# Performance work log

Measured on AMD Instinct MI355X. Metric: run time of the kernel, lower is better.

Reference implementation:

```python
import jax, jax.numpy as jnp
import numpy as np

B, N, D = 2, 2048, 1024
H = 16
HD = D // H
SCALE = HD ** -0.5


def setup_inputs() -> dict:
    key = jax.random.key(0)
    k1, k2, kw, kb = jax.random.split(key, 4)
    x1 = jax.random.normal(k1, (B, N, D), dtype=jnp.float32)
    x2 = jax.random.normal(k2, (B, N, D), dtype=jnp.float32)
    # fused qkv linear: torch nn.Linear(dim, 3*dim): W [3D, D], b [3D]
    bound = 1.0 / np.sqrt(D)
    qkv_w = jax.random.uniform(kw, (3 * D, D), minval=-bound, maxval=bound, dtype=jnp.float32)
    qkv_b = jax.random.uniform(kb, (3 * D,), minval=-bound, maxval=bound, dtype=jnp.float32)
    return {"x1": x1, "x2": x2, "qkv_w": qkv_w, "qkv_b": qkv_b}


def reference(x1, x2, qkv_w, qkv_b):
    # qkv projections (only q from x1 and k,v from x2 are used by the module)
    q1 = (jnp.einsum('bnd,ed->bne', x1, qkv_w[:D]) + qkv_b[:D])
    k2 = (jnp.einsum('bnd,ed->bne', x2, qkv_w[D:2 * D]) + qkv_b[D:2 * D])
    v2 = (jnp.einsum('bnd,ed->bne', x2, qkv_w[2 * D:]) + qkv_b[2 * D:])
    # [B, H, N, HD]
    q1 = q1.reshape(B, N, H, HD).transpose(0, 2, 1, 3)
    k2 = k2.reshape(B, N, H, HD).transpose(0, 2, 1, 3)
    v2 = v2.reshape(B, N, H, HD).transpose(0, 2, 1, 3)
    # explicit QK^T -> softmax -> AV (materializes [B,H,N,N] like the original)
    scores = jnp.einsum('bhqd,bhkd->bhqk', q1, k2) * SCALE
    attn = jax.nn.softmax(scores, axis=-1)
    out = jnp.einsum('bhqk,bhkd->bhqd', attn, v2)
    # [B, N, D]; note original module skips out_proj (never applied in forward)
    return out.transpose(0, 2, 1, 3).reshape(B, N, D)
```

## Files before the change

kernel.cpp:

```cpp
#include <hip/hip_runtime.h>
#include <cstdint>
#include <cstddef>

#define B_   2
#define N_   2048
#define D_   1024
#define H_   16
#define HD_  64
#define QSCALE_ 0.18033688011112042f

typedef unsigned short u16;
typedef unsigned int   u32;
typedef __attribute__((ext_vector_type(8))) short short8;
typedef __attribute__((ext_vector_type(4))) float f32x4;
typedef __attribute__((ext_vector_type(16))) float f32x16;
typedef __attribute__((ext_vector_type(4))) float fl4;
typedef __attribute__((ext_vector_type(4))) unsigned short us4;
typedef __attribute__((ext_vector_type(4))) unsigned int u32x4;

#if __has_builtin(__builtin_amdgcn_exp2f)
#define EXP2F(x) __builtin_amdgcn_exp2f(x)
#else
#define EXP2F(x) exp2f(x)
#endif

__device__ __forceinline__ u16 f2bf(float f) {
  u32 u = __builtin_bit_cast(u32, f);
  u += 0x7fffu + ((u >> 16) & 1u);
  return (u16)(u >> 16);
}

__device__ __forceinline__ u32 cvtpk(float lo, float hi) {
  u32 r;
  asm("v_cvt_pk_bf16_f32 %0, %1, %2" : "=v"(r) : "v"(lo), "v"(hi));
  return r;
}

__device__ __forceinline__ void plswap(u32& a, u32& b) {
  asm volatile("v_permlane32_swap_b32 %0, %1" : "+v"(a), "+v"(b));
}

__device__ __forceinline__ void gload16(const void* g, void* l) {
  typedef __attribute__((address_space(1))) unsigned int gu32;
  typedef __attribute__((address_space(3))) unsigned int lu32;
  __builtin_amdgcn_global_load_lds((gu32*)g, (lu32*)l, 16, 0, 0);
}

__global__ void convert_kernel(const fl4* __restrict__ x1, const fl4* __restrict__ x2,
                               const fl4* __restrict__ w,
                               us4* __restrict__ o1, us4* __restrict__ o2,
                               us4* __restrict__ ow) {
  const int NX = (B_ * N_ * D_) / 4;
  const int NW = (3 * D_ * D_) / 4;
  int stride = gridDim.x * blockDim.x;
  for (int i = blockIdx.x * blockDim.x + threadIdx.x; i < NX; i += stride) {
    fl4 a = x1[i];
    us4 r; r.x = f2bf(a.x); r.y = f2bf(a.y); r.z = f2bf(a.z); r.w = f2bf(a.w);
    o1[i] = r;
    fl4 b = x2[i];
    us4 s; s.x = f2bf(b.x); s.y = f2bf(b.y); s.z = f2bf(b.z); s.w = f2bf(b.w);
    o2[i] = s;
    if (i < NW) {
      fl4 c = w[i];
      us4 t; t.x = f2bf(c.x); t.y = f2bf(c.y); t.z = f2bf(c.z); t.w = f2bf(c.w);
      ow[i] = t;
    }
  }
}

__global__ __launch_bounds__(256) void qkv_gemm(
    const u16* __restrict__ x1b, const u16* __restrict__ x2b,
    const u16* __restrict__ wb, const float* __restrict__ bias,
    u16* __restrict__ Qb, u16* __restrict__ Kb, u16* __restrict__ Vtb) {
  const int z = blockIdx.z;
  const u16* X = (z == 0) ? x1b : x2b;
  const u16* W = wb + (size_t)z * D_ * D_;
  const float* bz = bias + z * D_;
  const int m0 = blockIdx.y * 128;
  const int e0 = blockIdx.x * 128;
  const int tid = threadIdx.x;
  const int lane = tid & 63;
  const int w = tid >> 6;
  const int wr = w >> 1, wc = w & 1;
  const int col = lane & 15, quad = lane >> 4;

  __shared__ __align__(16) u16 As[128 * 32];
  __shared__ __align__(16) u16 Bs[128 * 32];

  f32x4 acc[4][4] = {};

  int off0 = w * 2048 + lane * 16;
  int row0 = off0 >> 6;
  int ke0  = (off0 & 63) >> 1;
  int off1 = off0 + 1024;
  int row1 = off1 >> 6;
  int ke1  = (off1 & 63) >> 1;

  const u16* gA0 = X + (size_t)(m0 + row0) * D_ + ke0;
  const u16* gA1 = X + (size_t)(m0 + row1) * D_ + ke1;
  const u16* gB0 = W + (size_t)(e0 + row0) * D_ + ke0;
  const u16* gB1 = W + (size_t)(e0 + row1) * D_ + ke1;
  u16* lA0 = &As[w * 1024];
  u16* lA1 = &As[w * 1024 + 512];
  u16* lB0 = &Bs[w * 1024];
  u16* lB1 = &Bs[w * 1024 + 512];

  for (int k0 = 0; k0 < D_; k0 += 32) {
    __syncthreads();
    gload16(gA0 + k0, lA0);
    gload16(gA1 + k0, lA1);
    gload16(gB0 + k0, lB0);
    gload16(gB1 + k0, lB1);
    __syncthreads();

    short8 a[4], b[4];
#pragma unroll
    for (int i = 0; i < 4; ++i)
      a[i] = *(const short8*)&As[(wr * 64 + i * 16 + col) * 32 + quad * 8];
#pragma unroll
    for (int j = 0; j < 4; ++j)
      b[j] = *(const short8*)&Bs[(wc * 64 + j * 16 + col) * 32 + quad * 8];
#pragma unroll
    for (int i = 0; i < 4; ++i)
#pragma unroll
      for (int j = 0; j < 4; ++j)
        acc[i][j] = __builtin_amdgcn_mfma_f32_16x16x32_bf16(a[i], b[j], acc[i][j], 0, 0, 0);
  }

#pragma unroll
  for (int j = 0; j < 4; ++j) {
    int eg = e0 + wc * 64 + j * 16 + col;
    float bj = bz[eg];
    int h = eg >> 6, d = eg & 63;
#pragma unroll
    for (int i = 0; i < 4; ++i) {
#pragma unroll
      for (int r = 0; r < 4; ++r) {
        int m = m0 + wr * 64 + i * 16 + quad * 4 + r;
        int bb = m >> 11, n = m & (N_ - 1);
        float v = acc[i][j][r] + bj;
        if (z == 0) v *= QSCALE_;
        u16 o = f2bf(v);
        if (z == 0)      Qb [(((size_t)bb * H_ + h) * N_ + n) * HD_ + d] = o;
        else if (z == 1) Kb [(((size_t)bb * H_ + h) * N_ + n) * HD_ + d] = o;
        else             Vtb[(((size_t)bb * H_ + h) * HD_ + d) * N_ + n] = o;
      }
    }
  }
}

__global__ __launch_bounds__(256, 2) void attn_kernel(
    const u16* __restrict__ Qb, const u16* __restrict__ Kb,
    const u16* __restrict__ Vtb, float* __restrict__ out) {
  const int bh = blockIdx.y;
  const int bb = bh >> 4, h = bh & 15;
  const int q0 = blockIdx.x * 128;
  const int tid = threadIdx.x;
  const int lane = tid & 63;
  const int w = tid >> 6;
  const int l31 = lane & 31, hf = lane >> 5, r7 = lane & 7;

  const u16* __restrict__ Q  = Qb  + ((size_t)bh << 17);
  const u16* __restrict__ K  = Kb  + ((size_t)bh << 17);
  const u16* __restrict__ Vt = Vtb + ((size_t)bh << 17);

  __shared__ __align__(16) u16 Ks[2][64 * 64];
  __shared__ __align__(16) u16 Vs[2][64 * 64];
  __shared__ float Ls[4][32];

  const u16* Qr = Q + (size_t)(q0 + w * 32 + l31) * HD_;
  short8 qf[4];
#pragma unroll
  for (int c = 0; c < 4; ++c)
    qf[c] = *(const short8*)&Qr[c * 16 + hf * 8];

  const int srow = tid >> 3;
  const int sg   = tid & 7;
  const int lw0 = srow * 64 + ((sg ^ (srow & 7)) * 8);
  const int lw1 = lw0 + 2048;
  const u16* gK = K + tid * 8;
  const u16* gV = Vt + srow * N_ + sg * 8;

  f32x16 accO[2] = {};
  float lsum = 0.f;

  short8 kA = *(const short8*)(gK);
  short8 kB = *(const short8*)(gK + 2048);
  short8 vA = *(const short8*)(gV);
  short8 vB = *(const short8*)(gV + 32 * N_);
  *(short8*)&Ks[0][lw0] = kA;
  *(short8*)&Ks[0][lw1] = kB;
  *(short8*)&Vs[0][lw0] = vA;
  *(short8*)&Vs[0][lw1] = vB;

  for (int t = 0; t < N_ / 64; ++t) {
    __syncthreads();
    const int cur = t & 1;
    if (t < N_ / 64 - 1) {
      const int k0n = (t + 1) * 64;
      kA = *(const short8*)(gK + k0n * 64);
      kB = *(const short8*)(gK + k0n * 64 + 2048);
      vA = *(const short8*)(gV + k0n);
      vB = *(const short8*)(gV + k0n + 32 * N_);
    }
    const u16* Kc = Ks[cur];
    const u16* Vc = Vs[cur];

    f32x16 sT[2] = {};
    __builtin_amdgcn_s_setprio(1);
#pragma unroll
    for (int kb = 0; kb < 2; ++kb) {
      const int rb = (kb * 32 + l31) * 64;
#pragma unroll
      for (int c = 0; c < 4; ++c) {
        short8 kf = *(const short8*)&Kc[rb + (((c * 2 + hf) ^ r7) * 8)];
        sT[kb] = __builtin_amdgcn_mfma_f32_32x32x16_bf16(kf, qf[c], sT[kb], 0, 0, 0);
      }
    }
    __builtin_amdgcn_s_setprio(0);

#pragma unroll
    for (int kb = 0; kb < 2; ++kb)
#pragma unroll
      for (int i = 0; i < 16; ++i) {
        float e = EXP2F(sT[kb][i]);
        lsum += e;
        sT[kb][i] = e;
      }

    short8 pf[4];
#pragma unroll
    for (int kc = 0; kc < 4; ++kc) {
      const int kb = kc >> 1, o = (kc & 1) * 8;
      u32 X = cvtpk(sT[kb][o + 0], sT[kb][o + 1]);
      u32 Y = cvtpk(sT[kb][o + 4], sT[kb][o + 5]);
      plswap(X, Y);
      u32 Z = cvtpk(sT[kb][o + 2], sT[kb][o + 3]);
      u32 W = cvtpk(sT[kb][o + 6], sT[kb][o + 7]);
      plswap(Z, W);
      u32x4 pw = {X, Z, Y, W};
      pf[kc] = __builtin_bit_cast(short8, pw);
    }

    __builtin_amdgcn_s_setprio(1);
#pragma unroll
    for (int db = 0; db < 2; ++db) {
      const int rb = (db * 32 + l31) * 64;
#pragma unroll
      for (int kc = 0; kc < 4; ++kc) {
        short8 vf = *(const short8*)&Vc[rb + (((kc * 2 + hf) ^ r7) * 8)];
        accO[db] = __builtin_amdgcn_mfma_f32_32x32x16_bf16(pf[kc], vf, accO[db], 0, 0, 0);
      }
    }
    __builtin_amdgcn_s_setprio(0);

    if (t < N_ / 64 - 1) {
      u16* Kn = (u16*)Ks[cur ^ 1];
      u16* Vn = (u16*)Vs[cur ^ 1];
      *(short8*)&Kn[lw0] = kA;
      *(short8*)&Kn[lw1] = kB;
      *(short8*)&Vn[lw0] = vA;
      *(short8*)&Vn[lw1] = vB;
    }
  }

  lsum += __shfl_xor(lsum, 32);
  if (hf == 0) Ls[w][l31] = 1.0f / lsum;
  __syncthreads();

  float rinv[16];
#pragma unroll
  for (int r = 0; r < 16; ++r)
    rinv[r] = Ls[w][(r & 3) + 8 * (r >> 2) + 4 * hf];

#pragma unroll
  for (int db = 0; db < 2; ++db)
#pragma unroll
    for (int r = 0; r < 16; ++r) {
      int n = q0 + w * 32 + (r & 3) + 8 * (r >> 2) + 4 * hf;
      int e = h * HD_ + db * 32 + l31;
      out[((size_t)bb * N_ + n) * D_ + e] = accO[db][r] * rinv[r];
    }
}

extern "C" void kernel_launch(void* const* d_in, const int* in_sizes, int n_in,
                              void* d_out, int out_size, void* d_ws, size_t ws_size,
                              hipStream_t stream) {
  const float* x1 = (const float*)d_in[0];
  const float* x2 = (const float*)d_in[1];
  const float* qw = (const float*)d_in[2];
  const float* qb = (const float*)d_in[3];
  float* out = (float*)d_out;

  u16* ws   = (u16*)d_ws;
  u16* x1b  = ws;
  u16* x2b  = ws + 4194304;
  u16* wb   = ws + 8388608;
  u16* Qbf  = ws + 11534336;
  u16* Kbf  = ws + 15728640;
  u16* Vtb  = ws + 19922944;
  if (ws_size < (size_t)24117248 * 2) return;

  convert_kernel<<<dim3(1024), dim3(256), 0, stream>>>(
      (const fl4*)x1, (const fl4*)x2, (const fl4*)qw,
      (us4*)x1b, (us4*)x2b, (us4*)wb);

  qkv_gemm<<<dim3(8, 32, 3), dim3(256), 0, stream>>>(
      x1b, x2b, wb, qb, Qbf, Kbf, Vtb);

  attn_kernel<<<dim3(16, 32), dim3(256), 0, stream>>>(Qbf, Kbf, Vtb, out);
}
```

Measured before the change: 172.1 us.

## Fuse fp32-to-bf16 conversion into QKV GEMM with register-staged double buffering

Removes the separate convert kernel and has the QKV GEMM read fp32 inputs and weights directly. Each tile is converted to bf16 in registers and written into a double-buffered LDS tile, with the next tile's global loads issued before the current MFMAs, and MFMA priority is raised via s_setprio. This drops a kernel launch and the write and re-read of the bf16 copies, and shrinks the workspace. In exchange each GEMM block now reads twice the bytes (fp32) and repeats the conversion for every tile reuse across blocks, and it replaces the async global_load_lds path with register staging.

```diff
diff --git a/kernel.cpp b/kernel.cpp
--- a/kernel.cpp
+++ b/kernel.cpp
@@ -36,45 +36,23 @@
   return r;
 }
 
+__device__ __forceinline__ short8 pack8(fl4 lo, fl4 hi) {
+  u32x4 r = { cvtpk(lo.x, lo.y), cvtpk(lo.z, lo.w),
+              cvtpk(hi.x, hi.y), cvtpk(hi.z, hi.w) };
+  return __builtin_bit_cast(short8, r);
+}
+
 __device__ __forceinline__ void plswap(u32& a, u32& b) {
   asm volatile("v_permlane32_swap_b32 %0, %1" : "+v"(a), "+v"(b));
 }
 
-__device__ __forceinline__ void gload16(const void* g, void* l) {
-  typedef __attribute__((address_space(1))) unsigned int gu32;
-  typedef __attribute__((address_space(3))) unsigned int lu32;
-  __builtin_amdgcn_global_load_lds((gu32*)g, (lu32*)l, 16, 0, 0);
-}
-
-__global__ void convert_kernel(const fl4* __restrict__ x1, const fl4* __restrict__ x2,
-                               const fl4* __restrict__ w,
-                               us4* __restrict__ o1, us4* __restrict__ o2,
-                               us4* __restrict__ ow) {
-  const int NX = (B_ * N_ * D_) / 4;
-  const int NW = (3 * D_ * D_) / 4;
-  int stride = gridDim.x * blockDim.x;
-  for (int i = blockIdx.x * blockDim.x + threadIdx.x; i < NX; i += stride) {
-    fl4 a = x1[i];
-    us4 r; r.x = f2bf(a.x); r.y = f2bf(a.y); r.z = f2bf(a.z); r.w = f2bf(a.w);
-    o1[i] = r;
-    fl4 b = x2[i];
-    us4 s; s.x = f2bf(b.x); s.y = f2bf(b.y); s.z = f2bf(b.z); s.w = f2bf(b.w);
-    o2[i] = s;
-    if (i < NW) {
-      fl4 c = w[i];
-      us4 t; t.x = f2bf(c.x); t.y = f2bf(c.y); t.z = f2bf(c.z); t.w = f2bf(c.w);
-      ow[i] = t;
-    }
-  }
-}
-
 __global__ __launch_bounds__(256) void qkv_gemm(
-    const u16* __restrict__ x1b, const u16* __restrict__ x2b,
-    const u16* __restrict__ wb, const float* __restrict__ bias,
+    const float* __restrict__ x1, const float* __restrict__ x2,
+    const float* __restrict__ qw, const float* __restrict__ bias,
     u16* __restrict__ Qb, u16* __restrict__ Kb, u16* __restrict__ Vtb) {
   const int z = blockIdx.z;
-  const u16* X = (z == 0) ? x1b : x2b;
-  const u16* W = wb + (size_t)z * D_ * D_;
+  const float* X = (z == 0) ? x1 : x2;
+  const float* W = qw + (size_t)z * D_ * D_;
   const float* bz = bias + z * D_;
   const int m0 = blockIdx.y * 128;
   const int e0 = blockIdx.x * 128;
@@ -84,48 +62,64 @@
   const int wr = w >> 1, wc = w & 1;
   const int col = lane & 15, quad = lane >> 4;
 
-  __shared__ __align__(16) u16 As[128 * 32];
-  __shared__ __align__(16) u16 Bs[128 * 32];
+  __shared__ __align__(16) u16 As[2][128 * 32];
+  __shared__ __align__(16) u16 Bs[2][128 * 32];
 
   f32x4 acc[4][4] = {};
 
-  int off0 = w * 2048 + lane * 16;
-  int row0 = off0 >> 6;
-  int ke0  = (off0 & 63) >> 1;
-  int off1 = off0 + 1024;
-  int row1 = off1 >> 6;
-  int ke1  = (off1 & 63) >> 1;
-
-  const u16* gA0 = X + (size_t)(m0 + row0) * D_ + ke0;
-  const u16* gA1 = X + (size_t)(m0 + row1) * D_ + ke1;
-  const u16* gB0 = W + (size_t)(e0 + row0) * D_ + ke0;
-  const u16* gB1 = W + (size_t)(e0 + row1) * D_ + ke1;
-  u16* lA0 = &As[w * 1024];
-  u16* lA1 = &As[w * 1024 + 512];
-  u16* lB0 = &Bs[w * 1024];
-  u16* lB1 = &Bs[w * 1024 + 512];
-
-  for (int k0 = 0; k0 < D_; k0 += 32) {
+  const int srow = tid >> 2;
+  const int seg  = tid & 3;
+  const float* gA0 = X + (size_t)(m0 + srow) * D_ + seg * 8;
+  const float* gA1 = X + (size_t)(m0 + 64 + srow) * D_ + seg * 8;
+  const float* gB0 = W + (size_t)(e0 + srow) * D_ + seg * 8;
+  const float* gB1 = W + (size_t)(e0 + 64 + srow) * D_ + seg * 8;
+  const int ls0 = srow * 32 + seg * 8;
+  const int ls1 = (srow + 64) * 32 + seg * 8;
+
+  fl4 aal, aah, abl, abh, bal, bah, bbl, bbh;
+
+#define LOADT(k0)                                                     \
+  do {                                                                \
+    aal = *(const fl4*)(gA0 + (k0)); aah = *(const fl4*)(gA0 + (k0) + 4); \
+    abl = *(const fl4*)(gA1 + (k0)); abh = *(const fl4*)(gA1 + (k0) + 4); \
+    bal = *(const fl4*)(gB0 + (k0)); bah = *(const fl4*)(gB0 + (k0) + 4); \
+    bbl = *(const fl4*)(gB1 + (k0)); bbh = *(const fl4*)(gB1 + (k0) + 4); \
+  } while (0)
+#define STORET(buf)                                                   \
+  do {                                                                \
+    *(short8*)&As[buf][ls0] = pack8(aal, aah);                        \
+    *(short8*)&As[buf][ls1] = pack8(abl, abh);                        \
+    *(short8*)&Bs[buf][ls0] = pack8(bal, bah);                        \
+    *(short8*)&Bs[buf][ls1] = pack8(bbl, bbh);                        \
+  } while (0)
+
+  LOADT(0);
+  STORET(0);
+
+  for (int t = 0; t < D_ / 32; ++t) {
     __syncthreads();
-    gload16(gA0 + k0, lA0);
-    gload16(gA1 + k0, lA1);
-    gload16(gB0 + k0, lB0);
-    gload16(gB1 + k0, lB1);
-    __syncthreads();
+    const int cur = t & 1;
+    if (t < D_ / 32 - 1) LOADT((t + 1) * 32);
 
     short8 a[4], b[4];
 #pragma unroll
     for (int i = 0; i < 4; ++i)
-      a[i] = *(const short8*)&As[(wr * 64 + i * 16 + col) * 32 + quad * 8];
+      a[i] = *(const short8*)&As[cur][(wr * 64 + i * 16 + col) * 32 + quad * 8];
 #pragma unroll
     for (int j = 0; j < 4; ++j)
-      b[j] = *(const short8*)&Bs[(wc * 64 + j * 16 + col) * 32 + quad * 8];
+      b[j] = *(const short8*)&Bs[cur][(wc * 64 + j * 16 + col) * 32 + quad * 8];
+    __builtin_amdgcn_s_setprio(1);
 #pragma unroll
     for (int i = 0; i < 4; ++i)
 #pragma unroll
       for (int j = 0; j < 4; ++j)
         acc[i][j] = __builtin_amdgcn_mfma_f32_16x16x32_bf16(a[i], b[j], acc[i][j], 0, 0, 0);
+    __builtin_amdgcn_s_setprio(0);
+
+    if (t < D_ / 32 - 1) STORET(cur ^ 1);
   }
+#undef LOADT
+#undef STORET
 
 #pragma unroll
   for (int j = 0; j < 4; ++j) {
@@ -293,20 +287,13 @@
   float* out = (float*)d_out;
 
   u16* ws   = (u16*)d_ws;
-  u16* x1b  = ws;
-  u16* x2b  = ws + 4194304;
-  u16* wb   = ws + 8388608;
-  u16* Qbf  = ws + 11534336;
-  u16* Kbf  = ws + 15728640;
-  u16* Vtb  = ws + 19922944;
-  if (ws_size < (size_t)24117248 * 2) return;
-
-  convert_kernel<<<dim3(1024), dim3(256), 0, stream>>>(
-      (const fl4*)x1, (const fl4*)x2, (const fl4*)qw,
-      (us4*)x1b, (us4*)x2b, (us4*)wb);
+  u16* Qbf  = ws;
+  u16* Kbf  = ws + 4194304;
+  u16* Vtb  = ws + 8388608;
+  if (ws_size < (size_t)12582912 * 2) return;
 
   qkv_gemm<<<dim3(8, 32, 3), dim3(256), 0, stream>>>(
-      x1b, x2b, wb, qb, Qbf, Kbf, Vtb);
+      x1, x2, qw, qb, Qbf, Kbf, Vtb);
 
   attn_kernel<<<dim3(16, 32), dim3(256), 0, stream>>>(Qbf, Kbf, Vtb, out);
 }
```

New measurement: 186.9 us. 8.6% more time.

## Double QKV GEMM K-tile to 64 with XOR-swizzled LDS layout and setprio

Applied to the files above, without the earlier changes.

The QKV projection GEMM now stages a 64-wide K slice per iteration instead of 32, which halves the number of barrier-separated load/compute rounds. Global-to-LDS loads use an XOR swizzle on the 8-element column group so that fragment reads avoid LDS bank conflicts. The MFMA block is wrapped in s_setprio to raise wave priority during compute. This costs twice the LDS per block, which could lower occupancy.

```diff
diff --git a/kernel.cpp b/kernel.cpp
--- a/kernel.cpp
+++ b/kernel.cpp
@@ -84,47 +84,50 @@
   const int wr = w >> 1, wc = w & 1;
   const int col = lane & 15, quad = lane >> 4;
 
-  __shared__ __align__(16) u16 As[128 * 32];
-  __shared__ __align__(16) u16 Bs[128 * 32];
+  __shared__ __align__(16) u16 As[128 * 64];
+  __shared__ __align__(16) u16 Bs[128 * 64];
 
   f32x4 acc[4][4] = {};
 
-  int off0 = w * 2048 + lane * 16;
-  int row0 = off0 >> 6;
-  int ke0  = (off0 & 63) >> 1;
-  int off1 = off0 + 1024;
-  int row1 = off1 >> 6;
-  int ke1  = (off1 & 63) >> 1;
-
-  const u16* gA0 = X + (size_t)(m0 + row0) * D_ + ke0;
-  const u16* gA1 = X + (size_t)(m0 + row1) * D_ + ke1;
-  const u16* gB0 = W + (size_t)(e0 + row0) * D_ + ke0;
-  const u16* gB1 = W + (size_t)(e0 + row1) * D_ + ke1;
-  u16* lA0 = &As[w * 1024];
-  u16* lA1 = &As[w * 1024 + 512];
-  u16* lB0 = &Bs[w * 1024];
-  u16* lB1 = &Bs[w * 1024 + 512];
-
-  for (int k0 = 0; k0 < D_; k0 += 32) {
+  const int cg = (lane & 7) ^ (lane >> 3);
+  const u16* sA = X + (size_t)(m0 + w * 8 + (lane >> 3)) * D_ + cg * 8;
+  const u16* sB = W + (size_t)(e0 + w * 8 + (lane >> 3)) * D_ + cg * 8;
+  u16* dA = &As[w * 512];
+  u16* dB = &Bs[w * 512];
+
+  const int pg = (quad ^ (col & 7)) * 8;
+
+  for (int k0 = 0; k0 < D_; k0 += 64) {
     __syncthreads();
-    gload16(gA0 + k0, lA0);
-    gload16(gA1 + k0, lA1);
-    gload16(gB0 + k0, lB0);
-    gload16(gB1 + k0, lB1);
+#pragma unroll
+    for (int rr = 0; rr < 4; ++rr) {
+      gload16(sA + (size_t)rr * 32 * D_ + k0, dA + rr * 2048);
+      gload16(sB + (size_t)rr * 32 * D_ + k0, dB + rr * 2048);
+    }
     __syncthreads();
 
-    short8 a[4], b[4];
+    short8 a[4][2], b[4][2];
+#pragma unroll
+    for (int i = 0; i < 4; ++i) {
+      const int rb = (wr * 64 + i * 16 + col) * 64;
+      a[i][0] = *(const short8*)&As[rb + pg];
+      a[i][1] = *(const short8*)&As[rb + (pg ^ 32)];
+    }
+#pragma unroll
+    for (int j = 0; j < 4; ++j) {
+      const int rb = (wc * 64 + j * 16 + col) * 64;
+      b[j][0] = *(const short8*)&Bs[rb + pg];
+      b[j][1] = *(const short8*)&Bs[rb + (pg ^ 32)];
+    }
+    __builtin_amdgcn_s_setprio(1);
 #pragma unroll
     for (int i = 0; i < 4; ++i)
-      a[i] = *(const short8*)&As[(wr * 64 + i * 16 + col) * 32 + quad * 8];
-#pragma unroll
-    for (int j = 0; j < 4; ++j)
-      b[j] = *(const short8*)&Bs[(wc * 64 + j * 16 + col) * 32 + quad * 8];
-#pragma unroll
-    for (int i = 0; i < 4; ++i)
-#pragma unroll
-      for (int j = 0; j < 4; ++j)
-        acc[i][j] = __builtin_amdgcn_mfma_f32_16x16x32_bf16(a[i], b[j], acc[i][j], 0, 0, 0);
+#pragma unroll
+      for (int j = 0; j < 4; ++j) {
+        acc[i][j] = __builtin_amdgcn_mfma_f32_16x16x32_bf16(a[i][0], b[j][0], acc[i][j], 0, 0, 0);
+        acc[i][j] = __builtin_amdgcn_mfma_f32_16x16x32_bf16(a[i][1], b[j][1], acc[i][j], 0, 0, 0);
+      }
+    __builtin_amdgcn_s_setprio(0);
   }
 
 #pragma unroll
```

After: 170.7 us, median of 3. No clear change (-0.8%).
